# Optimization experiments

Measured on AMD Instinct MI355X. Metric: run time of the kernel, lower is better.

## Reference

```python
import jax, jax.numpy as jnp
import numpy as np

B, C_IN, N = 8, 512, 4096   # batch, input channels, timesteps
D, K = 256, 2048            # code dim (n_out), codebook size (vq_n_embed)
EMA_G = 0.99                # vq_ema_gamma


def setup_inputs() -> dict:
    key = jax.random.key(0)
    k1, k2, k3 = jax.random.split(key, 3)
    z = jax.random.normal(k1, (B, C_IN, N), jnp.float32)
    # emb: xavier_uniform with gain=10 over (K, D)
    eb = 10.0 * np.sqrt(6.0 / (K + D))
    emb = jax.random.uniform(k2, (K, D), jnp.float32, -eb, eb)
    # 1x1 Conv1d weight (no bias), xavier_uniform over (D, C_IN)
    wb = np.sqrt(6.0 / (D + C_IN))
    W = jax.random.uniform(k3, (D, C_IN), jnp.float32, -wb, wb)
    # EMA buffers as initialized in __init__
    ema_numer = emb * (1.0 - EMA_G)
    ema_denom = jnp.ones((K,), jnp.float32) * (1.0 - EMA_G)
    return {"z": z, "W": W, "emb": emb, "ema_numer": ema_numer, "ema_denom": ema_denom}


def reference(z, W, emb, ema_numer, ema_denom):
    # 1x1 conv (no bias): ze (B, D, N)
    ze = jnp.einsum('dc,bcn->bdn', W, z)
    e = jax.lax.stop_gradient(emb)  # sg(emb)
    # Squared L2 distances (B, K, N) via ||ze||^2 + ||e||^2 - 2 e.ze
    # (mathematically equal to the broadcasted (ze-e)^2 sum, without the
    #  huge (B,K,D,N) intermediate)
    ze_sq = jnp.sum(ze * ze, axis=1)              # (B, N)
    e_sq = jnp.sum(e * e, axis=1)                 # (K,)
    cross = jnp.einsum('kd,bdn->bkn', e, ze)      # (B, K, N)
    d2 = ze_sq[:, None, :] + e_sq[None, :, None] - 2.0 * cross
    min_ind = jnp.argmin(d2, axis=1)              # (B, N) int
    zq = jnp.take(e, min_ind, axis=0).transpose(0, 2, 1)  # (B, D, N)
    # ReplaceGrad straight-through: value = zq, gradient flows to ze
    out = ze + jax.lax.stop_gradient(zq - ze)
    # EMA codebook statistics (scatter-add over assignments)
    flat_ind = min_ind.reshape(-1)                          # (B*N,)
    flat_ze = ze.transpose(0, 2, 1).reshape(-1, D)          # (B*N, D)
    z_sum = jax.ops.segment_sum(flat_ze, flat_ind, num_segments=K)
    n_sum = jax.ops.segment_sum(jnp.ones((flat_ind.shape[0],), ze.dtype), flat_ind, num_segments=K)
    ema_numer_new = EMA_G * ema_numer + (1.0 - EMA_G) * z_sum
    ema_denom_new = EMA_G * ema_denom + (1.0 - EMA_G) * n_sum
    return out, ema_numer_new, ema_denom_new
```

## Files before the change

### kernel.cpp

```cpp
#include <hip/hip_runtime.h>

#define B_   8
#define CIN  512
#define NN_  4096
#define DD   256
#define KK   2048
#define KSPLIT 4
#define KPER (KK / KSPLIT)
#define NG   (B_ * NN_)

typedef _Float16 f16x8 __attribute__((ext_vector_type(8)));
typedef _Float16 f16x4 __attribute__((ext_vector_type(4)));
typedef float    f32x16 __attribute__((ext_vector_type(16)));

#define MFMA16 __builtin_amdgcn_mfma_f32_32x32x16_f16

#define GLDS16(gp, lp) __builtin_amdgcn_global_load_lds( \
    (const __attribute__((address_space(1))) void*)(gp), \
    (__attribute__((address_space(3))) void*)(lp), 16, 0, 0)

__global__ __launch_bounds__(256) void k_esq(const float* __restrict__ emb,
                                             float* __restrict__ esq,
                                             _Float16* __restrict__ emb_h,
                                             _Float16* __restrict__ emb_l) {
  int t = threadIdx.x;
  int lane = t & 63;
  int k = blockIdx.x * 4 + (t >> 6);
  float4 v = *(const float4*)&emb[(size_t)k * DD + 4 * lane];
  float s = v.x * v.x + v.y * v.y + v.z * v.z + v.w * v.w;
  f16x4 h, l;
  float* vp = (float*)&v;
#pragma unroll
  for (int i = 0; i < 4; i++) {
    _Float16 hh = (_Float16)vp[i];
    h[i] = hh;
    l[i] = (_Float16)(vp[i] - (float)hh);
  }
  *(f16x4*)&emb_h[(size_t)k * DD + 4 * lane] = h;
  *(f16x4*)&emb_l[(size_t)k * DD + 4 * lane] = l;
  for (int off = 32; off > 0; off >>= 1) s += __shfl_down(s, off, 64);
  if (lane == 0) esq[k] = s;
}

__global__ __launch_bounds__(256) void k_ze(const float* __restrict__ W,
                                            const float* __restrict__ z,
                                            _Float16* __restrict__ zeT_h,
                                            _Float16* __restrict__ zeT_l) {
  __shared__ __align__(16) char sm[69632];
  const int t = threadIdx.x;
  const int w = t >> 6, lane = t & 63;
  const int lr = lane & 31, lh = lane >> 5;
  const int wm = w & 1, wn = w >> 1;
  const int swz = (lr >> 1) & 3;
  const int b = blockIdx.z, d0 = blockIdx.y * 128, n0 = blockIdx.x * 128;

  auto stageA = [&](int buf, int c0) {
    _Float16* Ah = (_Float16*)(sm + buf * 8192);
    _Float16* Al = (_Float16*)(sm + 16384 + buf * 8192);
#pragma unroll
    for (int i = 0; i < 4; i++) {
      int fid = i * 256 + t;
      int d = fid >> 3, q8 = fid & 7;
      float4 v = *(const float4*)&W[(size_t)(d0 + d) * CIN + c0 + 4 * q8];
      float* vp = (float*)&v;
      f16x4 h, l;
#pragma unroll
      for (int e = 0; e < 4; e++) {
        _Float16 hh = (_Float16)vp[e];
        h[e] = hh;
        l[e] = (_Float16)(vp[e] - (float)hh);
      }
      int p16 = (q8 >> 1) ^ ((d >> 1) & 3);
      int off = d * 32 + p16 * 8 + (q8 & 1) * 4;
      *(f16x4*)&Ah[off] = h;
      *(f16x4*)&Al[off] = l;
    }
  };

  auto stageZ = [&](int buf, int c0) {
    const int n_l = t & 127, cg = t >> 7;
    const float* gp = z + ((size_t)b * CIN + c0 + cg * 16) * NN_ + n0 + n_l;
    float v[16];
#pragma unroll
    for (int j = 0; j < 16; j++) v[j] = gp[(size_t)j * NN_];
    _Float16* Zh = (_Float16*)(sm + 32768 + buf * 8192);
    _Float16* Zl = (_Float16*)(sm + 49152 + buf * 8192);
#pragma unroll
    for (int q = 0; q < 2; q++) {
      f16x8 h, l;
#pragma unroll
      for (int e = 0; e < 8; e++) {
        float x = v[q * 8 + e];
        _Float16 hh = (_Float16)x;
        h[e] = hh;
        l[e] = (_Float16)(x - (float)hh);
      }
      int p = (cg * 2 + q) ^ ((n_l >> 1) & 3);
      *(f16x8*)&Zh[n_l * 32 + p * 8] = h;
      *(f16x8*)&Zl[n_l * 32 + p * 8] = l;
    }
  };

  f32x16 acc[2][2];
#pragma unroll
  for (int mt = 0; mt < 2; mt++)
#pragma unroll
    for (int nt = 0; nt < 2; nt++)
#pragma unroll
      for (int i = 0; i < 16; i++) acc[mt][nt][i] = 0.0f;

  stageA(0, 0);
  stageZ(0, 0);
  int buf = 0;
  for (int c0 = 0; c0 < CIN; c0 += 32) {
    __syncthreads();
    if (c0 + 32 < CIN) { stageA(buf ^ 1, c0 + 32); stageZ(buf ^ 1, c0 + 32); }
    const _Float16* WhB = (const _Float16*)(sm + buf * 8192);
    const _Float16* WlB = (const _Float16*)(sm + 16384 + buf * 8192);
    const _Float16* ZhB = (const _Float16*)(sm + 32768 + buf * 8192);
    const _Float16* ZlB = (const _Float16*)(sm + 49152 + buf * 8192);
#pragma unroll
    for (int s = 0; s < 2; s++) {
      const int p = (2 * s + lh) ^ swz;
      const int acol = p * 8;
      const int ar0 = (wm * 64 + lr) * 32 + acol;
      const int ar1 = (wm * 64 + 32 + lr) * 32 + acol;
      const int br0 = (wn * 64 + lr) * 32 + acol;
      const int br1 = (wn * 64 + 32 + lr) * 32 + acol;
      f16x8 ah0 = *(const f16x8*)(WhB + ar0);
      f16x8 ah1 = *(const f16x8*)(WhB + ar1);
      f16x8 al0 = *(const f16x8*)(WlB + ar0);
      f16x8 al1 = *(const f16x8*)(WlB + ar1);
      f16x8 bh0 = *(const f16x8*)(ZhB + br0);
      f16x8 bh1 = *(const f16x8*)(ZhB + br1);
      f16x8 bl0 = *(const f16x8*)(ZlB + br0);
      f16x8 bl1 = *(const f16x8*)(ZlB + br1);
      acc[0][0] = MFMA16(ah0, bh0, acc[0][0], 0, 0, 0);
      acc[0][1] = MFMA16(ah0, bh1, acc[0][1], 0, 0, 0);
      acc[1][0] = MFMA16(ah1, bh0, acc[1][0], 0, 0, 0);
      acc[1][1] = MFMA16(ah1, bh1, acc[1][1], 0, 0, 0);
      acc[0][0] = MFMA16(ah0, bl0, acc[0][0], 0, 0, 0);
      acc[0][1] = MFMA16(ah0, bl1, acc[0][1], 0, 0, 0);
      acc[1][0] = MFMA16(ah1, bl0, acc[1][0], 0, 0, 0);
      acc[1][1] = MFMA16(ah1, bl1, acc[1][1], 0, 0, 0);
      acc[0][0] = MFMA16(al0, bh0, acc[0][0], 0, 0, 0);
      acc[0][1] = MFMA16(al0, bh1, acc[0][1], 0, 0, 0);
      acc[1][0] = MFMA16(al1, bh0, acc[1][0], 0, 0, 0);
      acc[1][1] = MFMA16(al1, bh1, acc[1][1], 0, 0, 0);
    }
    buf ^= 1;
  }

  __syncthreads();
  _Float16* Eh = (_Float16*)sm;
  _Float16* El = (_Float16*)(sm + 33792);
#pragma unroll
  for (int mt = 0; mt < 2; mt++)
#pragma unroll
    for (int nt = 0; nt < 2; nt++) {
      int n_l = wn * 64 + nt * 32 + lr;
#pragma unroll
      for (int g = 0; g < 4; g++) {
        int d_l = wm * 64 + mt * 32 + 8 * g + 4 * lh;
        f16x4 h, l;
#pragma unroll
        for (int e = 0; e < 4; e++) {
          float x = acc[mt][nt][4 * g + e];
          _Float16 hh = (_Float16)x;
          h[e] = hh;
          l[e] = (_Float16)(x - (float)hh);
        }
        *(f16x4*)&Eh[n_l * 132 + d_l] = h;
        *(f16x4*)&El[n_l * 132 + d_l] = l;
      }
    }
  __syncthreads();
  _Float16* gh = zeT_h + ((size_t)b * NN_ + n0) * DD + d0;
  _Float16* gl = zeT_l + ((size_t)b * NN_ + n0) * DD + d0;
#pragma unroll
  for (int i = 0; i < 16; i++) {
    int n = i * 8 + w * 2 + lh;
    int d = 4 * lr;
    *(f16x4*)&gh[(size_t)n * DD + d] = *(const f16x4*)&Eh[n * 132 + d];
    *(f16x4*)&gl[(size_t)n * DD + d] = *(const f16x4*)&El[n * 132 + d];
  }
}

__global__ __launch_bounds__(256) void k_argmin(const _Float16* __restrict__ emb_h,
                                                const _Float16* __restrict__ emb_l,
                                                const _Float16* __restrict__ zeT_h,
                                                const _Float16* __restrict__ zeT_l,
                                                const float* __restrict__ esq,
                                                float* __restrict__ pval,
                                                int* __restrict__ pidx) {
  __shared__ __align__(16) char sm[69632];
  const int t = threadIdx.x;
  const int w = t >> 6, lane = t & 63;
  const int lr = lane & 31, lh = lane >> 5;
  const int wm = w & 1, wn = w >> 1;
  const int swz = (lr >> 1) & 3;
  const int b = blockIdx.y, n0 = blockIdx.x * 128, ks = blockIdx.z;
  const int kbase = ks * KPER;

  float* esqs = (float*)(sm + 65536);
  *(float2*)&esqs[2 * t] = *(const float2*)&esq[kbase + 2 * t];

  const _Float16* zb_h = zeT_h + ((size_t)b * NN_ + n0) * DD;
  const _Float16* zb_l = zeT_l + ((size_t)b * NN_ + n0) * DD;

  auto stage = [&](int buf, int kt, int dc) {
    const int k0 = kbase + kt * 128;
    const int q = lane & 3, rr = lane >> 2;
    const int g = q ^ ((rr >> 1) & 3);
    const int rb0 = 32 * w;
#pragma unroll
    for (int j = 0; j < 2; j++) {
      int rb = rb0 + 16 * j;
      int r = rb + rr;
      int col = dc + 8 * g;
      size_t eo = (size_t)(k0 + r) * DD + col;
      size_t zo = (size_t)r * DD + col;
      char* lb = sm + (size_t)buf * 8192 + rb * 64;
      GLDS16(emb_h + eo, lb);
      GLDS16(emb_l + eo, lb + 16384);
      GLDS16(zb_h + zo, lb + 32768);
      GLDS16(zb_l + zo, lb + 49152);
    }
  };

  f32x16 vzero;
#pragma unroll
  for (int i = 0; i < 16; i++) vzero[i] = 0.0f;

  float bestv[2];
  int   besti[2];
  bestv[0] = bestv[1] = 3.4e38f;
  besti[0] = besti[1] = 0;

  stage(0, 0, 0);
  int buf = 0;
  for (int kt = 0; kt < 4; kt++) {
    f32x16 acc00 = vzero, acc01 = vzero, acc10 = vzero, acc11 = vzero;
    for (int dc = 0; dc < DD; dc += 32) {
      __syncthreads();
      if (dc + 32 < DD) stage(buf ^ 1, kt, dc + 32);
      else if (kt < 3) stage(buf ^ 1, kt + 1, 0);
      const _Float16* EHb = (const _Float16*)(sm + buf * 8192);
      const _Float16* ELb = (const _Float16*)(sm + 16384 + buf * 8192);
      const _Float16* ZHb = (const _Float16*)(sm + 32768 + buf * 8192);
      const _Float16* ZLb = (const _Float16*)(sm + 49152 + buf * 8192);
#pragma unroll
      for (int s = 0; s < 2; s++) {
        const int p = (2 * s + lh) ^ swz;
        const int acol = p * 8;
        const int ar0 = (wm * 64 + lr) * 32 + acol;
        const int ar1 = (wm * 64 + 32 + lr) * 32 + acol;
        const int br0 = (wn * 64 + lr) * 32 + acol;
        const int br1 = (wn * 64 + 32 + lr) * 32 + acol;
        f16x8 ah0 = *(const f16x8*)(EHb + ar0);
        f16x8 ah1 = *(const f16x8*)(EHb + ar1);
        f16x8 al0 = *(const f16x8*)(ELb + ar0);
        f16x8 al1 = *(const f16x8*)(ELb + ar1);
        f16x8 bh0 = *(const f16x8*)(ZHb + br0);
        f16x8 bh1 = *(const f16x8*)(ZHb + br1);
        f16x8 bl0 = *(const f16x8*)(ZLb + br0);
        f16x8 bl1 = *(const f16x8*)(ZLb + br1);
        acc00 = MFMA16(ah0, bh0, acc00, 0, 0, 0);
        acc01 = MFMA16(ah0, bh1, acc01, 0, 0, 0);
        acc10 = MFMA16(ah1, bh0, acc10, 0, 0, 0);
        acc11 = MFMA16(ah1, bh1, acc11, 0, 0, 0);
        acc00 = MFMA16(ah0, bl0, acc00, 0, 0, 0);
        acc01 = MFMA16(ah0, bl1, acc01, 0, 0, 0);
        acc10 = MFMA16(ah1, bl0, acc10, 0, 0, 0);
        acc11 = MFMA16(ah1, bl1, acc11, 0, 0, 0);
        acc00 = MFMA16(al0, bh0, acc00, 0, 0, 0);
        acc01 = MFMA16(al0, bh1, acc01, 0, 0, 0);
        acc10 = MFMA16(al1, bh0, acc10, 0, 0, 0);
        acc11 = MFMA16(al1, bh1, acc11, 0, 0, 0);
      }
      buf ^= 1;
    }
#pragma unroll
    for (int mt = 0; mt < 2; mt++)
#pragma unroll
      for (int nt = 0; nt < 2; nt++) {
        const f32x16& a = (mt == 0) ? (nt == 0 ? acc00 : acc01)
                                    : (nt == 0 ? acc10 : acc11);
#pragma unroll
        for (int r = 0; r < 16; r++) {
          int kl = kt * 128 + wm * 64 + mt * 32 + (r & 3) + 8 * (r >> 2) + 4 * lh;
          float d2 = esqs[kl] - 2.0f * a[r];
          int kg = kbase + kl;
          if (d2 < bestv[nt] || (d2 == bestv[nt] && kg < besti[nt])) {
            bestv[nt] = d2; besti[nt] = kg;
          }
        }
      }
  }

#pragma unroll
  for (int nt = 0; nt < 2; nt++) {
    float ov = __shfl_xor(bestv[nt], 32, 64);
    int   oi = __shfl_xor(besti[nt], 32, 64);
    if (ov < bestv[nt] || (ov == bestv[nt] && oi < besti[nt])) {
      bestv[nt] = ov; besti[nt] = oi;
    }
  }
  float* pv = (float*)(sm + 67584);
  int*   pi = (int*)(sm + 68608);
  __syncthreads();
  if (lh == 0) {
#pragma unroll
    for (int nt = 0; nt < 2; nt++) {
      pv[(w * 2 + nt) * 32 + lr] = bestv[nt];
      pi[(w * 2 + nt) * 32 + lr] = besti[nt];
    }
  }
  __syncthreads();
  if (t < 128) {
    int wn2 = t >> 6, nt = (t >> 5) & 1, nl = t & 31;
    int i0 = ((2 * wn2 + 0) * 2 + nt) * 32 + nl;
    int i1 = ((2 * wn2 + 1) * 2 + nt) * 32 + nl;
    float v0 = pv[i0], v1 = pv[i1];
    int   j0 = pi[i0], j1 = pi[i1];
    if (v1 < v0 || (v1 == v0 && j1 < j0)) { v0 = v1; j0 = j1; }
    size_t o = ((size_t)ks * B_ + b) * NN_ + n0 + t;
    pval[o] = v0;
    pidx[o] = j0;
  }
}

__global__ __launch_bounds__(256) void k_histm(const float* __restrict__ pval,
                                               const int* __restrict__ pidx,
                                               int* __restrict__ mind,
                                               int* __restrict__ hist) {
  __shared__ int h[KK];
  const int t = threadIdx.x;
#pragma unroll
  for (int i = 0; i < 8; i++) h[t + 256 * i] = 0;
  __syncthreads();
  const int base = blockIdx.x * 2048;
#pragma unroll
  for (int i = 0; i < 8; i++) {
    int g = base + i * 256 + t;
    float bv = pval[g];
    int   bi = pidx[g];
#pragma unroll
    for (int ks = 1; ks < KSPLIT; ks++) {
      float v = pval[(size_t)ks * NG + g];
      int  ii = pidx[(size_t)ks * NG + g];
      if (v < bv || (v == bv && ii < bi)) { bv = v; bi = ii; }
    }
    mind[g] = bi;
    atomicAdd(&h[bi], 1);
  }
  __syncthreads();
#pragma unroll
  for (int i = 0; i < 8; i++) {
    int v = h[t + 256 * i];
    if (v) atomicAdd(&hist[t + 256 * i], v);
  }
}

__global__ __launch_bounds__(256) void k_scan(const int* __restrict__ hist,
                                              int* __restrict__ cursor,
                                              float* __restrict__ nsumf) {
  __shared__ int ps[256];
  const int t = threadIdx.x;
  int c[8], s = 0;
#pragma unroll
  for (int e = 0; e < 8; e++) { c[e] = hist[8 * t + e]; s += c[e]; }
  ps[t] = s;
  __syncthreads();
  for (int off = 1; off < 256; off <<= 1) {
    int v = (t >= off) ? ps[t - off] : 0;
    __syncthreads();
    ps[t] += v;
    __syncthreads();
  }
  int run = ps[t] - s;
#pragma unroll
  for (int e = 0; e < 8; e++) {
    cursor[8 * t + e] = run;
    nsumf[8 * t + e] = (float)c[e];
    run += c[e];
  }
}

__global__ __launch_bounds__(256) void k_pos(const int* __restrict__ mind,
                                             int* __restrict__ cursor,
                                             int* __restrict__ sortp) {
  int g = blockIdx.x * 256 + threadIdx.x;
  int k = mind[g];
  int p = atomicAdd(&cursor[k], 1);
  sortp[p] = (k << 15) | g;
}

__global__ __launch_bounds__(256) void k_out(const float* __restrict__ emb,
                                             const int* __restrict__ mind,
                                             float* __restrict__ out) {
  __shared__ __align__(16) float E[64][257];
  __shared__ int idxl[64];
  const int t = threadIdx.x;
  const int b  = blockIdx.y;
  const int n0 = blockIdx.x * 64;
  if (t < 64) idxl[t] = mind[(size_t)b * NN_ + n0 + t];
  __syncthreads();

  for (int i = 0; i < 16; i++) {
    int cid = t + 256 * i;
    int r = cid >> 6, q = cid & 63;
    float4 v = *(const float4*)&emb[(size_t)idxl[r] * DD + 4 * q];
    float* vp = (float*)&v;
    E[r][4 * q + 0] = vp[0];
    E[r][4 * q + 1] = vp[1];
    E[r][4 * q + 2] = vp[2];
    E[r][4 * q + 3] = vp[3];
  }
  __syncthreads();
  const int nq = t & 15, dg = t >> 4;
  float* outb = out + (size_t)b * DD * NN_ + n0;
#pragma unroll
  for (int i = 0; i < 16; i++) {
    int d = i * 16 + dg;
    float4 v = make_float4(E[4 * nq + 0][d], E[4 * nq + 1][d],
                           E[4 * nq + 2][d], E[4 * nq + 3][d]);
    *(float4*)&outb[(size_t)d * NN_ + 4 * nq] = v;
  }
}

__global__ __launch_bounds__(256) void k_zsum(const int* __restrict__ sortp,
                                              const _Float16* __restrict__ zeT_h,
                                              const _Float16* __restrict__ zeT_l,
                                              float* __restrict__ z_sum) {
  __shared__ int sg[256];
  const int t = threadIdx.x;
  const int w = t >> 6, lane = t & 63;
  sg[t] = sortp[blockIdx.x * 256 + t];
  __syncthreads();
  const int base = w * 64;
  float acc[4] = {0.f, 0.f, 0.f, 0.f};
  int cur = sg[base] >> 15;
  for (int j = 0; j < 64; j++) {
    int e = sg[base + j];
    int k = e >> 15, g = e & 32767;
    if (k != cur) {
      float* zs = &z_sum[(size_t)cur * DD + 4 * lane];
#pragma unroll
      for (int x = 0; x < 4; x++) { atomicAdd(&zs[x], acc[x]); acc[x] = 0.f; }
      cur = k;
    }
    f16x4 h = *(const f16x4*)&zeT_h[(size_t)g * DD + 4 * lane];
    f16x4 l = *(const f16x4*)&zeT_l[(size_t)g * DD + 4 * lane];
#pragma unroll
    for (int x = 0; x < 4; x++) acc[x] += (float)h[x] + (float)l[x];
  }
  float* zs = &z_sum[(size_t)cur * DD + 4 * lane];
#pragma unroll
  for (int x = 0; x < 4; x++) atomicAdd(&zs[x], acc[x]);
}

__global__ __launch_bounds__(256) void k_ema(const float* __restrict__ ema_numer,
                                             const float* __restrict__ ema_denom,
                                             const float* __restrict__ z_sum,
                                             const float* __restrict__ nsumf,
                                             float* __restrict__ out_numer,
                                             float* __restrict__ out_denom) {
  const float G  = 0.99f;
  const float OG = 0.009999999776482582f;
  int i = blockIdx.x * 256 + threadIdx.x;
  if (i < KK * DD) {
    out_numer[i] = G * ema_numer[i] + OG * z_sum[i];
  } else {
    int j = i - KK * DD;
    if (j < KK) out_denom[j] = G * ema_denom[j] + OG * nsumf[j];
  }
}

extern "C" void kernel_launch(void* const* d_in, const int* in_sizes, int n_in,
                              void* d_out, int out_size, void* d_ws, size_t ws_size,
                              hipStream_t stream) {
  (void)in_sizes; (void)n_in; (void)out_size; (void)ws_size;
  const float* z         = (const float*)d_in[0];
  const float* W         = (const float*)d_in[1];
  const float* emb       = (const float*)d_in[2];
  const float* ema_numer = (const float*)d_in[3];
  const float* ema_denom = (const float*)d_in[4];

  float* out       = (float*)d_out;
  float* out_numer = out + (size_t)B_ * DD * NN_;
  float* out_denom = out_numer + (size_t)KK * DD;

  const size_t ZET = (size_t)B_ * NN_ * DD;
  _Float16* zeT_h = (_Float16*)d_ws;
  _Float16* zeT_l = zeT_h + ZET;
  float* esq    = (float*)(zeT_l + ZET);
  float* zsum   = esq + KK;
  int*   hist   = (int*)(zsum + (size_t)KK * DD);
  int*   cursor = hist + KK;
  float* nsumf  = (float*)(cursor + KK);
  float* pval   = nsumf + KK;
  int*   pidx   = (int*)(pval + (size_t)KSPLIT * NG);
  int*   mind   = pidx + (size_t)KSPLIT * NG;
  int*   sortp  = mind + NG;
  _Float16* emb_h = (_Float16*)(sortp + NG);
  _Float16* emb_l = emb_h + (size_t)KK * DD;

  hipMemsetAsync(zsum, 0, (size_t)(KK * DD + KK) * sizeof(float), stream);

  k_esq<<<dim3(KK / 4), 256, 0, stream>>>(emb, esq, emb_h, emb_l);
  k_ze<<<dim3(NN_ / 128, DD / 128, B_), 256, 0, stream>>>(W, z, zeT_h, zeT_l);
  k_argmin<<<dim3(NN_ / 128, B_, KSPLIT), 256, 0, stream>>>(emb_h, emb_l, zeT_h, zeT_l,
                                                            esq, pval, pidx);
  k_histm<<<dim3(NG / 2048), 256, 0, stream>>>(pval, pidx, mind, hist);
  k_scan<<<dim3(1), 256, 0, stream>>>(hist, cursor, nsumf);
  k_pos<<<dim3(NG / 256), 256, 0, stream>>>(mind, cursor, sortp);
  k_out<<<dim3(NN_ / 64, B_), 256, 0, stream>>>(emb, mind, out);
  k_zsum<<<dim3(NG / 256), 256, 0, stream>>>(sortp, zeT_h, zeT_l, zsum);
  k_ema<<<dim3((KK * DD + KK) / 256), 256, 0, stream>>>(ema_numer, ema_denom, zsum, nsumf,
                                                        out_numer, out_denom);
}
```

Measured before the change: 309.1 us.

## Pre-split W and z into transposed fp16 hi/lo buffers, stage via global_load_lds

W is now converted to fp16 hi/lo once inside the codebook prep kernel, and a new transpose kernel writes z as (B,N,C) fp16 hi/lo planes, using the output buffer as scratch for one of them. The projection GEMM then fills shared memory with direct global-to-LDS 16-byte loads and no longer converts or does strided scalar loads. This removes the per-block register staging and repeated fp32 conversion of W and z. The cost is an extra pass over z (reading fp32, writing two fp16 copies) and an extra kernel launch.

```diff
diff --git a/kernel.cpp b/kernel.cpp
--- a/kernel.cpp
+++ b/kernel.cpp
@@ -20,9 +20,12 @@
     (__attribute__((address_space(3))) void*)(lp), 16, 0, 0)
 
 __global__ __launch_bounds__(256) void k_esq(const float* __restrict__ emb,
+                                             const float* __restrict__ W,
                                              float* __restrict__ esq,
                                              _Float16* __restrict__ emb_h,
-                                             _Float16* __restrict__ emb_l) {
+                                             _Float16* __restrict__ emb_l,
+                                             _Float16* __restrict__ w_h,
+                                             _Float16* __restrict__ w_l) {
   int t = threadIdx.x;
   int lane = t & 63;
   int k = blockIdx.x * 4 + (t >> 6);
@@ -38,15 +41,58 @@
   }
   *(f16x4*)&emb_h[(size_t)k * DD + 4 * lane] = h;
   *(f16x4*)&emb_l[(size_t)k * DD + 4 * lane] = l;
+  int gi = blockIdx.x * 256 + t;
+  float wv = W[gi];
+  _Float16 wh = (_Float16)wv;
+  w_h[gi] = wh;
+  w_l[gi] = (_Float16)(wv - (float)wh);
   for (int off = 32; off > 0; off >>= 1) s += __shfl_down(s, off, 64);
   if (lane == 0) esq[k] = s;
 }
 
-__global__ __launch_bounds__(256) void k_ze(const float* __restrict__ W,
-                                            const float* __restrict__ z,
+__global__ __launch_bounds__(256) void k_zt(const float* __restrict__ z,
+                                            _Float16* __restrict__ zt_h,
+                                            _Float16* __restrict__ zt_l) {
+  __shared__ __align__(16) float E[64][68];
+  const int t = threadIdx.x;
+  const int b = blockIdx.z, c0 = blockIdx.y * 64, n0 = blockIdx.x * 64;
+  {
+    const int c_l = t >> 2, nq = t & 3;
+    const float* gp = &z[((size_t)b * CIN + c0 + c_l) * NN_ + n0 + nq * 16];
+#pragma unroll
+    for (int j = 0; j < 4; j++) {
+      float4 v = *(const float4*)&gp[4 * j];
+      *(float4*)&E[c_l][nq * 16 + 4 * j] = v;
+    }
+  }
+  __syncthreads();
+  {
+    const int n_l = t >> 2, cg = t & 3;
+    f16x8 h[2], l[2];
+#pragma unroll
+    for (int q = 0; q < 2; q++)
+#pragma unroll
+      for (int e = 0; e < 8; e++) {
+        float x = E[cg * 16 + q * 8 + e][n_l];
+        _Float16 hh = (_Float16)x;
+        h[q][e] = hh;
+        l[q][e] = (_Float16)(x - (float)hh);
+      }
+    size_t o = ((size_t)b * NN_ + n0 + n_l) * CIN + c0 + cg * 16;
+    *(f16x8*)&zt_h[o] = h[0];
+    *(f16x8*)&zt_h[o + 8] = h[1];
+    *(f16x8*)&zt_l[o] = l[0];
+    *(f16x8*)&zt_l[o + 8] = l[1];
+  }
+}
+
+__global__ __launch_bounds__(256) void k_ze(const _Float16* __restrict__ w_h,
+                                            const _Float16* __restrict__ w_l,
+                                            const _Float16* __restrict__ zt_h,
+                                            const _Float16* __restrict__ zt_l,
                                             _Float16* __restrict__ zeT_h,
                                             _Float16* __restrict__ zeT_l) {
-  __shared__ __align__(16) char sm[69632];
+  __shared__ __align__(16) char sm[67584];
   const int t = threadIdx.x;
   const int w = t >> 6, lane = t & 63;
   const int lr = lane & 31, lh = lane >> 5;
@@ -54,53 +100,28 @@
   const int swz = (lr >> 1) & 3;
   const int b = blockIdx.z, d0 = blockIdx.y * 128, n0 = blockIdx.x * 128;
 
-  auto stageA = [&](int buf, int c0) {
-    _Float16* Ah = (_Float16*)(sm + buf * 8192);
-    _Float16* Al = (_Float16*)(sm + 16384 + buf * 8192);
-#pragma unroll
-    for (int i = 0; i < 4; i++) {
-      int fid = i * 256 + t;
-      int d = fid >> 3, q8 = fid & 7;
-      float4 v = *(const float4*)&W[(size_t)(d0 + d) * CIN + c0 + 4 * q8];
-      float* vp = (float*)&v;
-      f16x4 h, l;
-#pragma unroll
-      for (int e = 0; e < 4; e++) {
-        _Float16 hh = (_Float16)vp[e];
-        h[e] = hh;
-        l[e] = (_Float16)(vp[e] - (float)hh);
-      }
-      int p16 = (q8 >> 1) ^ ((d >> 1) & 3);
-      int off = d * 32 + p16 * 8 + (q8 & 1) * 4;
-      *(f16x4*)&Ah[off] = h;
-      *(f16x4*)&Al[off] = l;
+  const _Float16* zb_h = zt_h + ((size_t)b * NN_ + n0) * CIN;
+  const _Float16* zb_l = zt_l + ((size_t)b * NN_ + n0) * CIN;
+
+  auto stage = [&](int buf, int c0) {
+    const int q = lane & 3, rr = lane >> 2;
+    const int g = q ^ ((rr >> 1) & 3);
+    const int rb0 = 32 * w;
+#pragma unroll
+    for (int j = 0; j < 2; j++) {
+      int rb = rb0 + 16 * j;
+      int r = rb + rr;
+      int col = c0 + 8 * g;
+      size_t wo = (size_t)(d0 + r) * CIN + col;
+      size_t zo = (size_t)r * CIN + col;
+      char* lb = sm + (size_t)buf * 8192 + rb * 64;
+      GLDS16(w_h + wo, lb);
+      GLDS16(w_l + wo, lb + 16384);
+      GLDS16(zb_h + zo, lb + 32768);
+      GLDS16(zb_l + zo, lb + 49152);
     }
   };
 
-  auto stageZ = [&](int buf, int c0) {
-    const int n_l = t & 127, cg = t >> 7;
-    const float* gp = z + ((size_t)b * CIN + c0 + cg * 16) * NN_ + n0 + n_l;
-    float v[16];
-#pragma unroll
-    for (int j = 0; j < 16; j++) v[j] = gp[(size_t)j * NN_];
-    _Float16* Zh = (_Float16*)(sm + 32768 + buf * 8192);
-    _Float16* Zl = (_Float16*)(sm + 49152 + buf * 8192);
-#pragma unroll
-    for (int q = 0; q < 2; q++) {
-      f16x8 h, l;
-#pragma unroll
-      for (int e = 0; e < 8; e++) {
-        float x = v[q * 8 + e];
-        _Float16 hh = (_Float16)x;
-        h[e] = hh;
-        l[e] = (_Float16)(x - (float)hh);
-      }
-      int p = (cg * 2 + q) ^ ((n_l >> 1) & 3);
-      *(f16x8*)&Zh[n_l * 32 + p * 8] = h;
-      *(f16x8*)&Zl[n_l * 32 + p * 8] = l;
-    }
-  };
-
   f32x16 acc[2][2];
 #pragma unroll
   for (int mt = 0; mt < 2; mt++)
@@ -109,12 +130,11 @@
 #pragma unroll
       for (int i = 0; i < 16; i++) acc[mt][nt][i] = 0.0f;
 
-  stageA(0, 0);
-  stageZ(0, 0);
+  stage(0, 0);
   int buf = 0;
   for (int c0 = 0; c0 < CIN; c0 += 32) {
     __syncthreads();
-    if (c0 + 32 < CIN) { stageA(buf ^ 1, c0 + 32); stageZ(buf ^ 1, c0 + 32); }
+    if (c0 + 32 < CIN) stage(buf ^ 1, c0 + 32);
     const _Float16* WhB = (const _Float16*)(sm + buf * 8192);
     const _Float16* WlB = (const _Float16*)(sm + 16384 + buf * 8192);
     const _Float16* ZhB = (const _Float16*)(sm + 32768 + buf * 8192);
@@ -492,6 +512,7 @@
   float* out_denom = out_numer + (size_t)KK * DD;
 
   const size_t ZET = (size_t)B_ * NN_ * DD;
+  const size_t ZTN = (size_t)B_ * NN_ * CIN;
   _Float16* zeT_h = (_Float16*)d_ws;
   _Float16* zeT_l = zeT_h + ZET;
   float* esq    = (float*)(zeT_l + ZET);
@@ -505,11 +526,17 @@
   int*   sortp  = mind + NG;
   _Float16* emb_h = (_Float16*)(sortp + NG);
   _Float16* emb_l = emb_h + (size_t)KK * DD;
+  _Float16* w_h   = emb_l + (size_t)KK * DD;
+  _Float16* w_l   = w_h + (size_t)DD * CIN;
+  _Float16* zt_l  = w_l + (size_t)DD * CIN;
+  _Float16* zt_h  = (_Float16*)out;
 
   hipMemsetAsync(zsum, 0, (size_t)(KK * DD + KK) * sizeof(float), stream);
 
-  k_esq<<<dim3(KK / 4), 256, 0, stream>>>(emb, esq, emb_h, emb_l);
-  k_ze<<<dim3(NN_ / 128, DD / 128, B_), 256, 0, stream>>>(W, z, zeT_h, zeT_l);
+  k_esq<<<dim3(KK / 4), 256, 0, stream>>>(emb, W, esq, emb_h, emb_l, w_h, w_l);
+  k_zt<<<dim3(NN_ / 64, CIN / 64, B_), 256, 0, stream>>>(z, zt_h, zt_l);
+  k_ze<<<dim3(NN_ / 128, DD / 128, B_), 256, 0, stream>>>(w_h, w_l, zt_h, zt_l,
+                                                          zeT_h, zeT_l);
   k_argmin<<<dim3(NN_ / 128, B_, KSPLIT), 256, 0, stream>>>(emb_h, emb_l, zeT_h, zeT_l,
                                                             esq, pval, pidx);
   k_histm<<<dim3(NG / 2048), 256, 0, stream>>>(pval, pidx, mind, hist);
```

Measured after the change: 324.3 us. 1.05x slower.

## Enlarge argmin MFMA tile to 256x256 with 8 waves and phased prefetch

Applied to the files above, without the earlier changes.

The distance-GEMM/argmin kernel moves from 256 threads on 128x128 tiles to 512 threads on 256 (codebook) x 256 (timestep) tiles, with KSPLIT doubled so each block covers the whole 256-code slice at once. That removes the per-128-code accumulator reset loop. Global-to-LDS loads are now split into four chunks interleaved with four MFMA phases, using explicit vmcnt waits, raw s_barrier and s_setprio around MFMA bursts. The aim is more operand reuse per LDS byte and better overlap of loads with matrix math. In exchange it uses about 136 KB of LDS (one block per CU), more accumulator registers, and twice as many partial results for the merge kernel to read.

```diff
diff --git a/kernel.cpp b/kernel.cpp
--- a/kernel.cpp
+++ b/kernel.cpp
@@ -5,7 +5,7 @@
 #define NN_  4096
 #define DD   256
 #define KK   2048
-#define KSPLIT 4
+#define KSPLIT 8
 #define KPER (KK / KSPLIT)
 #define NG   (B_ * NN_)
 
@@ -186,118 +186,165 @@
   }
 }
 
-__global__ __launch_bounds__(256) void k_argmin(const _Float16* __restrict__ emb_h,
-                                                const _Float16* __restrict__ emb_l,
-                                                const _Float16* __restrict__ zeT_h,
-                                                const _Float16* __restrict__ zeT_l,
-                                                const float* __restrict__ esq,
-                                                float* __restrict__ pval,
-                                                int* __restrict__ pidx) {
-  __shared__ __align__(16) char sm[69632];
+__global__ __launch_bounds__(512, 2) void k_argmin(const _Float16* __restrict__ emb_h,
+                                                   const _Float16* __restrict__ emb_l,
+                                                   const _Float16* __restrict__ zeT_h,
+                                                   const _Float16* __restrict__ zeT_l,
+                                                   const float* __restrict__ esq,
+                                                   float* __restrict__ pval,
+                                                   int* __restrict__ pidx) {
+  __shared__ __align__(16) char sm[136192];
   const int t = threadIdx.x;
   const int w = t >> 6, lane = t & 63;
   const int lr = lane & 31, lh = lane >> 5;
   const int wm = w & 1, wn = w >> 1;
   const int swz = (lr >> 1) & 3;
-  const int b = blockIdx.y, n0 = blockIdx.x * 128, ks = blockIdx.z;
+  const int b = blockIdx.y, n0 = blockIdx.x * 256, ks = blockIdx.z;
   const int kbase = ks * KPER;
 
-  float* esqs = (float*)(sm + 65536);
-  *(float2*)&esqs[2 * t] = *(const float2*)&esq[kbase + 2 * t];
-
-  const _Float16* zb_h = zeT_h + ((size_t)b * NN_ + n0) * DD;
-  const _Float16* zb_l = zeT_l + ((size_t)b * NN_ + n0) * DD;
-
-  auto stage = [&](int buf, int kt, int dc) {
-    const int k0 = kbase + kt * 128;
-    const int q = lane & 3, rr = lane >> 2;
-    const int g = q ^ ((rr >> 1) & 3);
-    const int rb0 = 32 * w;
-#pragma unroll
-    for (int j = 0; j < 2; j++) {
-      int rb = rb0 + 16 * j;
-      int r = rb + rr;
-      int col = dc + 8 * g;
-      size_t eo = (size_t)(k0 + r) * DD + col;
-      size_t zo = (size_t)r * DD + col;
-      char* lb = sm + (size_t)buf * 8192 + rb * 64;
-      GLDS16(emb_h + eo, lb);
-      GLDS16(emb_l + eo, lb + 16384);
-      GLDS16(zb_h + zo, lb + 32768);
-      GLDS16(zb_l + zo, lb + 49152);
-    }
+  float* esqs = (float*)(sm + 131072);
+  if (t < 64) *(float4*)&esqs[4 * t] = *(const float4*)&esq[kbase + 4 * t];
+
+  const _Float16* srcp[4][2];
+#pragma unroll
+  for (int i = 0; i < 2; i++) {
+    int slot = i * 512 + t;
+    int row = slot >> 2;
+    int c = (slot & 3) ^ ((row >> 1) & 3);
+    size_t eo = (size_t)(kbase + row) * DD + 8 * c;
+    size_t zo = ((size_t)b * NN_ + n0 + row) * DD + 8 * c;
+    srcp[0][i] = emb_h + eo;
+    srcp[1][i] = emb_l + eo;
+    srcp[2][i] = zeT_h + zo;
+    srcp[3][i] = zeT_l + zo;
+  }
+  const int ldsw = w * 1024;
+  auto stageOp = [&](int T1, int j) {
+    GLDS16(srcp[j >> 1][j & 1] + T1 * 32,
+           sm + (T1 & 1) * 65536 + (j >> 1) * 16384 + (j & 1) * 8192 + ldsw);
   };
 
-  f32x16 vzero;
-#pragma unroll
-  for (int i = 0; i < 16; i++) vzero[i] = 0.0f;
+  f32x16 acc[4][2];
+#pragma unroll
+  for (int mt = 0; mt < 4; mt++)
+#pragma unroll
+    for (int nt = 0; nt < 2; nt++)
+#pragma unroll
+      for (int i = 0; i < 16; i++) acc[mt][nt][i] = 0.0f;
+
+#pragma unroll
+  for (int j = 0; j < 8; j++) stageOp(0, j);
+
+  const int arow = wm * 128 + lr;
+  const int brow = wn * 64 + lr;
+
+#pragma unroll 2
+  for (int T = 0; T < 8; T++) {
+    const char* bb = sm + (T & 1) * 65536;
+    const char* EhB = bb;
+    const char* ElB = bb + 16384;
+    const char* ZhB = bb + 32768;
+    const char* ZlB = bb + 49152;
+    f16x8 ah[4], al[4];
+
+    if (T < 7) {
+      stageOp(T + 1, 0); stageOp(T + 1, 1);
+      asm volatile("s_waitcnt vmcnt(2)" ::: "memory");
+    } else {
+      asm volatile("s_waitcnt vmcnt(0)" ::: "memory");
+    }
+    __builtin_amdgcn_s_barrier();
+    {
+      const int c0 = ((lh ^ swz) & 3) * 16;
+#pragma unroll
+      for (int mt = 0; mt < 4; mt++) {
+        ah[mt] = *(const f16x8*)(EhB + (arow + mt * 32) * 64 + c0);
+        al[mt] = *(const f16x8*)(ElB + (arow + mt * 32) * 64 + c0);
+      }
+      f16x8 bh = *(const f16x8*)(ZhB + brow * 64 + c0);
+      f16x8 bl = *(const f16x8*)(ZlB + brow * 64 + c0);
+      __builtin_amdgcn_s_setprio(1);
+#pragma unroll
+      for (int mt = 0; mt < 4; mt++) acc[mt][0] = MFMA16(ah[mt], bh, acc[mt][0], 0, 0, 0);
+#pragma unroll
+      for (int mt = 0; mt < 4; mt++) acc[mt][0] = MFMA16(ah[mt], bl, acc[mt][0], 0, 0, 0);
+#pragma unroll
+      for (int mt = 0; mt < 4; mt++) acc[mt][0] = MFMA16(al[mt], bh, acc[mt][0], 0, 0, 0);
+      __builtin_amdgcn_s_setprio(0);
+      __builtin_amdgcn_s_barrier();
+    }
+    {
+      const int c0 = ((lh ^ swz) & 3) * 16;
+      f16x8 bh = *(const f16x8*)(ZhB + (brow + 32) * 64 + c0);
+      f16x8 bl = *(const f16x8*)(ZlB + (brow + 32) * 64 + c0);
+      if (T < 7) { stageOp(T + 1, 2); stageOp(T + 1, 3); }
+      __builtin_amdgcn_s_barrier();
+      __builtin_amdgcn_s_setprio(1);
+#pragma unroll
+      for (int mt = 0; mt < 4; mt++) acc[mt][1] = MFMA16(ah[mt], bh, acc[mt][1], 0, 0, 0);
+#pragma unroll
+      for (int mt = 0; mt < 4; mt++) acc[mt][1] = MFMA16(ah[mt], bl, acc[mt][1], 0, 0, 0);
+#pragma unroll
+      for (int mt = 0; mt < 4; mt++) acc[mt][1] = MFMA16(al[mt], bh, acc[mt][1], 0, 0, 0);
+      __builtin_amdgcn_s_setprio(0);
+      __builtin_amdgcn_s_barrier();
+    }
+    {
+      const int c1 = (((2 + lh) ^ swz) & 3) * 16;
+#pragma unroll
+      for (int mt = 0; mt < 4; mt++) {
+        ah[mt] = *(const f16x8*)(EhB + (arow + mt * 32) * 64 + c1);
+        al[mt] = *(const f16x8*)(ElB + (arow + mt * 32) * 64 + c1);
+      }
+      f16x8 bh = *(const f16x8*)(ZhB + brow * 64 + c1);
+      f16x8 bl = *(const f16x8*)(ZlB + brow * 64 + c1);
+      if (T < 7) { stageOp(T + 1, 4); stageOp(T + 1, 5); }
+      __builtin_amdgcn_s_barrier();
+      __builtin_amdgcn_s_setprio(1);
+#pragma unroll
+      for (int mt = 0; mt < 4; mt++) acc[mt][0] = MFMA16(ah[mt], bh, acc[mt][0], 0, 0, 0);
+#pragma unroll
+      for (int mt = 0; mt < 4; mt++) acc[mt][0] = MFMA16(ah[mt], bl, acc[mt][0], 0, 0, 0);
+#pragma unroll
+      for (int mt = 0; mt < 4; mt++) acc[mt][0] = MFMA16(al[mt], bh, acc[mt][0], 0, 0, 0);
+      __builtin_amdgcn_s_setprio(0);
+      __builtin_amdgcn_s_barrier();
+    }
+    {
+      const int c1 = (((2 + lh) ^ swz) & 3) * 16;
+      f16x8 bh = *(const f16x8*)(ZhB + (brow + 32) * 64 + c1);
+      f16x8 bl = *(const f16x8*)(ZlB + (brow + 32) * 64 + c1);
+      if (T < 7) { stageOp(T + 1, 6); stageOp(T + 1, 7); }
+      __builtin_amdgcn_s_barrier();
+      __builtin_amdgcn_s_setprio(1);
+#pragma unroll
+      for (int mt = 0; mt < 4; mt++) acc[mt][1] = MFMA16(ah[mt], bh, acc[mt][1], 0, 0, 0);
+#pragma unroll
+      for (int mt = 0; mt < 4; mt++) acc[mt][1] = MFMA16(ah[mt], bl, acc[mt][1], 0, 0, 0);
+#pragma unroll
+      for (int mt = 0; mt < 4; mt++) acc[mt][1] = MFMA16(al[mt], bh, acc[mt][1], 0, 0, 0);
+      __builtin_amdgcn_s_setprio(0);
+      __builtin_amdgcn_s_barrier();
+    }
+  }
 
   float bestv[2];
   int   besti[2];
   bestv[0] = bestv[1] = 3.4e38f;
   besti[0] = besti[1] = 0;
-
-  stage(0, 0, 0);
-  int buf = 0;
-  for (int kt = 0; kt < 4; kt++) {
-    f32x16 acc00 = vzero, acc01 = vzero, acc10 = vzero, acc11 = vzero;
-    for (int dc = 0; dc < DD; dc += 32) {
-      __syncthreads();
-      if (dc + 32 < DD) stage(buf ^ 1, kt, dc + 32);
-      else if (kt < 3) stage(buf ^ 1, kt + 1, 0);
-      const _Float16* EHb = (const _Float16*)(sm + buf * 8192);
-      const _Float16* ELb = (const _Float16*)(sm + 16384 + buf * 8192);
-      const _Float16* ZHb = (const _Float16*)(sm + 32768 + buf * 8192);
-      const _Float16* ZLb = (const _Float16*)(sm + 49152 + buf * 8192);
-#pragma unroll
-      for (int s = 0; s < 2; s++) {
-        const int p = (2 * s + lh) ^ swz;
-        const int acol = p * 8;
-        const int ar0 = (wm * 64 + lr) * 32 + acol;
-        const int ar1 = (wm * 64 + 32 + lr) * 32 + acol;
-        const int br0 = (wn * 64 + lr) * 32 + acol;
-        const int br1 = (wn * 64 + 32 + lr) * 32 + acol;
-        f16x8 ah0 = *(const f16x8*)(EHb + ar0);
-        f16x8 ah1 = *(const f16x8*)(EHb + ar1);
-        f16x8 al0 = *(const f16x8*)(ELb + ar0);
-        f16x8 al1 = *(const f16x8*)(ELb + ar1);
-        f16x8 bh0 = *(const f16x8*)(ZHb + br0);
-        f16x8 bh1 = *(const f16x8*)(ZHb + br1);
-        f16x8 bl0 = *(const f16x8*)(ZLb + br0);
-        f16x8 bl1 = *(const f16x8*)(ZLb + br1);
-        acc00 = MFMA16(ah0, bh0, acc00, 0, 0, 0);
-        acc01 = MFMA16(ah0, bh1, acc01, 0, 0, 0);
-        acc10 = MFMA16(ah1, bh0, acc10, 0, 0, 0);
-        acc11 = MFMA16(ah1, bh1, acc11, 0, 0, 0);
-        acc00 = MFMA16(ah0, bl0, acc00, 0, 0, 0);
-        acc01 = MFMA16(ah0, bl1, acc01, 0, 0, 0);
-        acc10 = MFMA16(ah1, bl0, acc10, 0, 0, 0);
-        acc11 = MFMA16(ah1, bl1, acc11, 0, 0, 0);
-        acc00 = MFMA16(al0, bh0, acc00, 0, 0, 0);
-        acc01 = MFMA16(al0, bh1, acc01, 0, 0, 0);
-        acc10 = MFMA16(al1, bh0, acc10, 0, 0, 0);
-        acc11 = MFMA16(al1, bh1, acc11, 0, 0, 0);
-      }
-      buf ^= 1;
-    }
-#pragma unroll
-    for (int mt = 0; mt < 2; mt++)
-#pragma unroll
-      for (int nt = 0; nt < 2; nt++) {
-        const f32x16& a = (mt == 0) ? (nt == 0 ? acc00 : acc01)
-                                    : (nt == 0 ? acc10 : acc11);
-#pragma unroll
-        for (int r = 0; r < 16; r++) {
-          int kl = kt * 128 + wm * 64 + mt * 32 + (r & 3) + 8 * (r >> 2) + 4 * lh;
-          float d2 = esqs[kl] - 2.0f * a[r];
-          int kg = kbase + kl;
-          if (d2 < bestv[nt] || (d2 == bestv[nt] && kg < besti[nt])) {
-            bestv[nt] = d2; besti[nt] = kg;
-          }
+#pragma unroll
+  for (int mt = 0; mt < 4; mt++)
+#pragma unroll
+    for (int nt = 0; nt < 2; nt++)
+#pragma unroll
+      for (int r = 0; r < 16; r++) {
+        int kl = wm * 128 + mt * 32 + (r & 3) + 8 * (r >> 2) + 4 * lh;
+        float d2 = esqs[kl] - 2.0f * acc[mt][nt][r];
+        int kg = kbase + kl;
+        if (d2 < bestv[nt] || (d2 == bestv[nt] && kg < besti[nt])) {
+          bestv[nt] = d2; besti[nt] = kg;
         }
       }
-  }
-
 #pragma unroll
   for (int nt = 0; nt < 2; nt++) {
     float ov = __shfl_xor(bestv[nt], 32, 64);
@@ -306,9 +353,8 @@
       bestv[nt] = ov; besti[nt] = oi;
     }
   }
-  float* pv = (float*)(sm + 67584);
-  int*   pi = (int*)(sm + 68608);
-  __syncthreads();
+  float* pv = (float*)(sm + 132096);
+  int*   pi = (int*)(sm + 134144);
   if (lh == 0) {
 #pragma unroll
     for (int nt = 0; nt < 2; nt++) {
@@ -317,10 +363,10 @@
     }
   }
   __syncthreads();
-  if (t < 128) {
+  if (t < 256) {
     int wn2 = t >> 6, nt = (t >> 5) & 1, nl = t & 31;
-    int i0 = ((2 * wn2 + 0) * 2 + nt) * 32 + nl;
-    int i1 = ((2 * wn2 + 1) * 2 + nt) * 32 + nl;
+    int i0 = ((wn2 * 2 + 0) * 2 + nt) * 32 + nl;
+    int i1 = ((wn2 * 2 + 1) * 2 + nt) * 32 + nl;
     float v0 = pv[i0], v1 = pv[i1];
     int   j0 = pi[i0], j1 = pi[i1];
     if (v1 < v0 || (v1 == v0 && j1 < j0)) { v0 = v1; j0 = j1; }
@@ -510,7 +556,7 @@
 
   k_esq<<<dim3(KK / 4), 256, 0, stream>>>(emb, esq, emb_h, emb_l);
   k_ze<<<dim3(NN_ / 128, DD / 128, B_), 256, 0, stream>>>(W, z, zeT_h, zeT_l);
-  k_argmin<<<dim3(NN_ / 128, B_, KSPLIT), 256, 0, stream>>>(emb_h, emb_l, zeT_h, zeT_l,
+  k_argmin<<<dim3(NN_ / 256, B_, KSPLIT), 512, 0, stream>>>(emb_h, emb_l, zeT_h, zeT_l,
                                                             esq, pval, pidx);
   k_histm<<<dim3(NG / 2048), 256, 0, stream>>>(pval, pidx, mind, hist);
   k_scan<<<dim3(1), 256, 0, stream>>>(hist, cursor, nsumf);
```

After: 335.9 us. +8.7%, slower.

## Fold EMA epilogue into init, scan and zsum; merge position pass into gather

Applied to the files above, without the earlier changes.

The memset and the separate EMA kernel are removed. A new init kernel writes G*ema_numer straight into the output and zeroes the histogram. k_zsum then atomically adds the scaled code sums into that output, and k_scan computes the new denominator directly. The k_pos scatter is merged into k_out, which cuts two launches and a full pass over z_sum. The cost is that the final numerator now depends on atomic accumulation on top of the pre-scaled value.

```diff
diff --git a/kernel.cpp b/kernel.cpp
--- a/kernel.cpp
+++ b/kernel.cpp
@@ -18,6 +18,14 @@
 #define GLDS16(gp, lp) __builtin_amdgcn_global_load_lds( \
     (const __attribute__((address_space(1))) void*)(gp), \
     (__attribute__((address_space(3))) void*)(lp), 16, 0, 0)
+
+__global__ __launch_bounds__(256) void k_init(const float* __restrict__ ema_numer,
+                                              float* __restrict__ out_numer,
+                                              int* __restrict__ hist) {
+  int i = blockIdx.x * 256 + threadIdx.x;
+  if (i < KK * DD) out_numer[i] = 0.99f * ema_numer[i];
+  else hist[i - KK * DD] = 0;
+}
 
 __global__ __launch_bounds__(256) void k_esq(const float* __restrict__ emb,
                                              float* __restrict__ esq,
@@ -363,8 +371,11 @@
 }
 
 __global__ __launch_bounds__(256) void k_scan(const int* __restrict__ hist,
+                                              const float* __restrict__ ema_denom,
                                               int* __restrict__ cursor,
-                                              float* __restrict__ nsumf) {
+                                              float* __restrict__ out_denom) {
+  const float G  = 0.99f;
+  const float OG = 0.009999999776482582f;
   __shared__ int ps[256];
   const int t = threadIdx.x;
   int c[8], s = 0;
@@ -382,23 +393,16 @@
 #pragma unroll
   for (int e = 0; e < 8; e++) {
     cursor[8 * t + e] = run;
-    nsumf[8 * t + e] = (float)c[e];
+    out_denom[8 * t + e] = G * ema_denom[8 * t + e] + OG * (float)c[e];
     run += c[e];
   }
 }
 
-__global__ __launch_bounds__(256) void k_pos(const int* __restrict__ mind,
+__global__ __launch_bounds__(256) void k_out(const float* __restrict__ emb,
+                                             const int* __restrict__ mind,
+                                             float* __restrict__ out,
                                              int* __restrict__ cursor,
                                              int* __restrict__ sortp) {
-  int g = blockIdx.x * 256 + threadIdx.x;
-  int k = mind[g];
-  int p = atomicAdd(&cursor[k], 1);
-  sortp[p] = (k << 15) | g;
-}
-
-__global__ __launch_bounds__(256) void k_out(const float* __restrict__ emb,
-                                             const int* __restrict__ mind,
-                                             float* __restrict__ out) {
   __shared__ __align__(16) float E[64][257];
   __shared__ int idxl[64];
   const int t = threadIdx.x;
@@ -406,6 +410,13 @@
   const int n0 = blockIdx.x * 64;
   if (t < 64) idxl[t] = mind[(size_t)b * NN_ + n0 + t];
   __syncthreads();
+
+  if (t < 64) {
+    int g = b * NN_ + n0 + t;
+    int k = idxl[t];
+    int p = atomicAdd(&cursor[k], 1);
+    sortp[p] = (k << 15) | g;
+  }
 
   for (int i = 0; i < 16; i++) {
     int cid = t + 256 * i;
@@ -432,7 +443,8 @@
 __global__ __launch_bounds__(256) void k_zsum(const int* __restrict__ sortp,
                                               const _Float16* __restrict__ zeT_h,
                                               const _Float16* __restrict__ zeT_l,
-                                              float* __restrict__ z_sum) {
+                                              float* __restrict__ out_numer) {
+  const float OG = 0.009999999776482582f;
   __shared__ int sg[256];
   const int t = threadIdx.x;
   const int w = t >> 6, lane = t & 63;
@@ -445,9 +457,9 @@
     int e = sg[base + j];
     int k = e >> 15, g = e & 32767;
     if (k != cur) {
-      float* zs = &z_sum[(size_t)cur * DD + 4 * lane];
-#pragma unroll
-      for (int x = 0; x < 4; x++) { atomicAdd(&zs[x], acc[x]); acc[x] = 0.f; }
+      float* zs = &out_numer[(size_t)cur * DD + 4 * lane];
+#pragma unroll
+      for (int x = 0; x < 4; x++) { atomicAdd(&zs[x], OG * acc[x]); acc[x] = 0.f; }
       cur = k;
     }
     f16x4 h = *(const f16x4*)&zeT_h[(size_t)g * DD + 4 * lane];
@@ -455,26 +467,9 @@
 #pragma unroll
     for (int x = 0; x < 4; x++) acc[x] += (float)h[x] + (float)l[x];
   }
-  float* zs = &z_sum[(size_t)cur * DD + 4 * lane];
-#pragma unroll
-  for (int x = 0; x < 4; x++) atomicAdd(&zs[x], acc[x]);
-}
-
-__global__ __launch_bounds__(256) void k_ema(const float* __restrict__ ema_numer,
-                                             const float* __restrict__ ema_denom,
-                                             const float* __restrict__ z_sum,
-                                             const float* __restrict__ nsumf,
-                                             float* __restrict__ out_numer,
-                                             float* __restrict__ out_denom) {
-  const float G  = 0.99f;
-  const float OG = 0.009999999776482582f;
-  int i = blockIdx.x * 256 + threadIdx.x;
-  if (i < KK * DD) {
-    out_numer[i] = G * ema_numer[i] + OG * z_sum[i];
-  } else {
-    int j = i - KK * DD;
-    if (j < KK) out_denom[j] = G * ema_denom[j] + OG * nsumf[j];
-  }
+  float* zs = &out_numer[(size_t)cur * DD + 4 * lane];
+#pragma unroll
+  for (int x = 0; x < 4; x++) atomicAdd(&zs[x], OG * acc[x]);
 }
 
 extern "C" void kernel_launch(void* const* d_in, const int* in_sizes, int n_in,
@@ -495,28 +490,22 @@
   _Float16* zeT_h = (_Float16*)d_ws;
   _Float16* zeT_l = zeT_h + ZET;
   float* esq    = (float*)(zeT_l + ZET);
-  float* zsum   = esq + KK;
-  int*   hist   = (int*)(zsum + (size_t)KK * DD);
+  int*   hist   = (int*)(esq + KK);
   int*   cursor = hist + KK;
-  float* nsumf  = (float*)(cursor + KK);
-  float* pval   = nsumf + KK;
+  float* pval   = (float*)(cursor + KK);
   int*   pidx   = (int*)(pval + (size_t)KSPLIT * NG);
   int*   mind   = pidx + (size_t)KSPLIT * NG;
   int*   sortp  = mind + NG;
   _Float16* emb_h = (_Float16*)(sortp + NG);
   _Float16* emb_l = emb_h + (size_t)KK * DD;
 
-  hipMemsetAsync(zsum, 0, (size_t)(KK * DD + KK) * sizeof(float), stream);
-
+  k_init<<<dim3((KK * DD + KK) / 256), 256, 0, stream>>>(ema_numer, out_numer, hist);
   k_esq<<<dim3(KK / 4), 256, 0, stream>>>(emb, esq, emb_h, emb_l);
   k_ze<<<dim3(NN_ / 128, DD / 128, B_), 256, 0, stream>>>(W, z, zeT_h, zeT_l);
   k_argmin<<<dim3(NN_ / 128, B_, KSPLIT), 256, 0, stream>>>(emb_h, emb_l, zeT_h, zeT_l,
                                                             esq, pval, pidx);
   k_histm<<<dim3(NG / 2048), 256, 0, stream>>>(pval, pidx, mind, hist);
-  k_scan<<<dim3(1), 256, 0, stream>>>(hist, cursor, nsumf);
-  k_pos<<<dim3(NG / 256), 256, 0, stream>>>(mind, cursor, sortp);
-  k_out<<<dim3(NN_ / 64, B_), 256, 0, stream>>>(emb, mind, out);
-  k_zsum<<<dim3(NG / 256), 256, 0, stream>>>(sortp, zeT_h, zeT_l, zsum);
-  k_ema<<<dim3((KK * DD + KK) / 256), 256, 0, stream>>>(ema_numer, ema_denom, zsum, nsumf,
-                                                        out_numer, out_denom);
-}
+  k_scan<<<dim3(1), 256, 0, stream>>>(hist, ema_denom, cursor, out_denom);
+  k_out<<<dim3(NN_ / 64, B_), 256, 0, stream>>>(emb, mind, out, cursor, sortp);
+  k_zsum<<<dim3(NG / 256), 256, 0, stream>>>(sortp, zeT_h, zeT_l, out_numer);
+}
```

New measurement: 304.1 us. Within noise of the previous version (-1.6%).
